# Performance work log

Measured on AMD Instinct MI355X. Metric: run time of the kernel, lower is better.

## Reference

```python
import jax, jax.numpy as jnp
import numpy as np

N = 25000   # num nodes
E = 500000  # num edges
B = 4       # num queries (batch)
D = 32      # hidden dim
R2 = 474    # doubled num_relation
L = 4       # num conv layers
EPS = 1e-6


def setup_inputs() -> dict:
    key = jax.random.key(0)
    ks = jax.random.split(key, 12)
    return {
        "node_in": jax.random.randint(ks[0], (E,), 0, N),
        "node_out": jax.random.randint(ks[1], (E,), 0, N),
        "relation": jax.random.randint(ks[2], (E,), 0, R2),
        "edge_weight": jnp.ones((E,), jnp.float32),
        "h_index": jax.random.randint(ks[3], (B,), 0, N),
        "r_index": jax.random.randint(ks[4], (B,), 0, R2),
        "query_embed": jax.random.normal(ks[5], (R2, D), jnp.float32) * 0.1,
        "rel_W": jax.random.normal(ks[6], (L, D, R2 * D), jnp.float32) * 0.05,
        "rel_b": jnp.zeros((L, R2 * D), jnp.float32),
        "lin_W": jax.random.normal(ks[7], (L, 13 * D, D), jnp.float32) * 0.05,
        "lin_b": jnp.zeros((L, D), jnp.float32),
        "mlp_W1": jax.random.normal(ks[8], (2 * D, 2 * D), jnp.float32) * 0.05,
        "mlp_b1": jnp.zeros((2 * D,), jnp.float32),
        "mlp_W2": jax.random.normal(ks[9], (2 * D, 1), jnp.float32) * 0.05,
        "mlp_b2": jnp.zeros((1,), jnp.float32),
    }


def _nbfnet(node_in, node_out, relation, h_index, r_index,
            edge_weight, query_embed, rel_W, rel_b, lin_W, lin_b,
            mlp_W1, mlp_b1, mlp_W2, mlp_b2):
    query = query_embed[r_index]                                   # [B, D]
    # boundary condition: query embedding placed at the head node of each query
    boundary = jnp.zeros((N, B, D), query.dtype).at[h_index, jnp.arange(B)].set(query)
    # append one self-entry per node (boundary message), as in the torch code
    node_out_ext = jnp.concatenate([node_out, jnp.arange(N)])      # [E+N]
    w_ext = jnp.concatenate([edge_weight, jnp.ones((N,), edge_weight.dtype)])[:, None, None]
    cnt = jax.ops.segment_sum(jnp.ones((E + N,), query.dtype), node_out_ext, N)[:, None, None]
    deg = jax.ops.segment_sum(edge_weight, node_out, N) + 1.0      # degree_out + 1, [N]
    scale = jnp.log(deg)
    scale = scale / scale.mean()
    scales = jnp.stack([jnp.ones_like(scale), scale, 1.0 / jnp.clip(scale, 0.01)], -1)  # [N,3]

    hidden = boundary
    for l in range(L):
        # dependent relation embeddings: [R2, B, D]
        rel_in = (query @ rel_W[l] + rel_b[l]).reshape(B, R2, D).transpose(1, 0, 2)
        # distmult message + boundary self-message: [E+N, B, D]
        msg = jnp.concatenate([rel_in[relation] * hidden[node_in], boundary], 0)
        mw = msg * w_ext
        mean = jax.ops.segment_sum(mw, node_out_ext, N) / cnt
        sq_mean = jax.ops.segment_sum(msg * mw, node_out_ext, N) / cnt
        mx = jax.ops.segment_max(mw, node_out_ext, N)
        mn = jax.ops.segment_min(mw, node_out_ext, N)
        std = jnp.sqrt(jnp.clip(sq_mean - mean * mean, EPS))
        feat = jnp.stack([mean, mx, mn, std], -1).reshape(N, B, 4 * D)   # PNA stats
        update = (feat[..., None] * scales[:, None, None, :]).reshape(N, B, 12 * D)
        hidden = jax.nn.relu(jnp.concatenate([hidden, update], -1) @ lin_W[l] + lin_b[l])

    feat = jnp.concatenate([hidden, jnp.broadcast_to(query[None], (N, B, D))], -1)  # [N,B,2D]
    h1 = jax.nn.relu(feat @ mlp_W1 + mlp_b1)
    score = (h1 @ mlp_W2 + mlp_b2)[..., 0]                          # [N, B]
    return score.T                                                  # [B, N]


def reference(node_in, node_out, relation, edge_weight, h_index, r_index,
              query_embed, rel_W, rel_b, lin_W, lin_b,
              mlp_W1, mlp_b1, mlp_W2, mlp_b2):
    return _nbfnet(node_in, node_out, relation, h_index, r_index,
                   edge_weight, query_embed, rel_W, rel_b, lin_W, lin_b,
                   mlp_W1, mlp_b1, mlp_W2, mlp_b2)
```

## Files before the change

kernel.cpp:

```cpp
#include <hip/hip_runtime.h>
#include <hip/hip_fp16.h>

#define NN  25000
#define EE  500000
#define BB  4
#define DD  32
#define LL  4
#define R2C 474
#define BD  128
#define THD 416
#define EPSF 1e-6f
#define WMH 13312
#define CAP 64

#define NEB    245
#define NWMB   208
#define NRELIN 948
#define NW1P   16

typedef _Float16 half8 __attribute__((ext_vector_type(8)));
typedef float    f32x4 __attribute__((ext_vector_type(4)));

__global__ __launch_bounds__(256) void build_setup_kernel(
    const int* __restrict__ node_in, const int* __restrict__ node_out,
    const int* __restrict__ relation, const float* __restrict__ ew,
    int* __restrict__ cnt, int2* __restrict__ ep,
    const float* __restrict__ linW, _Float16* __restrict__ Wm,
    const int* __restrict__ r_index, const float* __restrict__ qemb,
    const float* __restrict__ relW, const float* __restrict__ relB,
    __half* __restrict__ relIn, float* __restrict__ query,
    const float* __restrict__ W1, _Float16* __restrict__ W1m) {
  const int blk = blockIdx.x;
  const int tid = threadIdx.x;
  if (blk < NEB) {
    int i = blk * 256 + tid;
    if (i >= EE / 8) return;
    const int4*   ni4 = (const int4*)node_in;
    const int4*   no4 = (const int4*)node_out;
    const int4*   rl4 = (const int4*)relation;
    const float4* ew4 = (const float4*)ew;
    int4   noA = no4[2 * i], noB = no4[2 * i + 1];
    int4   niA = ni4[2 * i], niB = ni4[2 * i + 1];
    int4   rlA = rl4[2 * i], rlB = rl4[2 * i + 1];
    float4 ewA = ew4[2 * i], ewB = ew4[2 * i + 1];
    int s0 = atomicAdd(&cnt[noA.x], 1);
    int s1 = atomicAdd(&cnt[noA.y], 1);
    int s2 = atomicAdd(&cnt[noA.z], 1);
    int s3 = atomicAdd(&cnt[noA.w], 1);
    int s4 = atomicAdd(&cnt[noB.x], 1);
    int s5 = atomicAdd(&cnt[noB.y], 1);
    int s6 = atomicAdd(&cnt[noB.z], 1);
    int s7 = atomicAdd(&cnt[noB.w], 1);
    ep[noA.x * CAP + s0] = make_int2(niA.x | (rlA.x << 15), __float_as_int(ewA.x));
    ep[noA.y * CAP + s1] = make_int2(niA.y | (rlA.y << 15), __float_as_int(ewA.y));
    ep[noA.z * CAP + s2] = make_int2(niA.z | (rlA.z << 15), __float_as_int(ewA.z));
    ep[noA.w * CAP + s3] = make_int2(niA.w | (rlA.w << 15), __float_as_int(ewA.w));
    ep[noB.x * CAP + s4] = make_int2(niB.x | (rlB.x << 15), __float_as_int(ewB.x));
    ep[noB.y * CAP + s5] = make_int2(niB.y | (rlB.y << 15), __float_as_int(ewB.y));
    ep[noB.z * CAP + s6] = make_int2(niB.z | (rlB.z << 15), __float_as_int(ewB.z));
    ep[noB.w * CAP + s7] = make_int2(niB.w | (rlB.w << 15), __float_as_int(ewB.w));
  } else if (blk < NEB + NWMB) {
    int idx = (blk - NEB) * 256 + tid;
    int l = idx / WMH, rest = idx % WMH;
    int t = rest >> 10;
    int nt = (rest >> 9) & 1;
    int L = (rest >> 3) & 63;
    int j = rest & 7;
    int k = t * 32 + (L >> 4) * 8 + j;
    int n = nt * 16 + (L & 15);
    int wrow;
    if (k < 32) wrow = k;
    else {
      int kk = k - 32;
      int slab = kk >> 7, s = (kk >> 5) & 3, dd = kk & 31;
      wrow = DD + (dd * 4 + s) * 3 + slab;
    }
    Wm[idx] = (_Float16)linW[(size_t)l * THD * DD + (size_t)wrow * DD + n];
  } else if (blk < NEB + NWMB + NRELIN) {
    int o = (blk - NEB - NWMB) * 256 + tid;
    int l = o / (R2C * BD);
    int rest = o % (R2C * BD);
    int r = rest >> 7, b = (rest >> 5) & 3, d = rest & 31;
    int col = r * DD + d;
    const float* W = relW + (size_t)l * DD * R2C * DD;
    const float* qrow = qemb + (size_t)r_index[b] * DD;
    float acc = relB[(size_t)l * R2C * DD + col];
    #pragma unroll
    for (int k = 0; k < DD; ++k)
      acc = fmaf(qrow[k], W[(size_t)k * (R2C * DD) + col], acc);
    relIn[o] = __float2half(acc);
  } else if (blk < NEB + NWMB + NRELIN + NW1P) {
    int idx = (blk - NEB - NWMB - NRELIN) * 256 + tid;
    int kc = idx >> 11;
    int nt = (idx >> 9) & 3;
    int L = (idx >> 3) & 63;
    int j = idx & 7;
    int k = kc * 32 + (L >> 4) * 8 + j;
    int c = nt * 16 + (L & 15);
    W1m[idx] = (_Float16)W1[(size_t)k * (2 * DD) + c];
  } else {
    if (tid < BD) query[tid] = qemb[(size_t)r_index[tid >> 5] * DD + (tid & 31)];
  }
}

__global__ __launch_bounds__(256) void lg_kernel(const int* __restrict__ cnt,
                                                 const int2* __restrict__ ep,
                                                 float* __restrict__ lg,
                                                 float* __restrict__ logsum) {
  int n = blockIdx.x * 256 + threadIdx.x;
  float v = 0.f;
  if (n < NN) {
    int c = cnt[n];
    const int2* seg = ep + (size_t)n * CAP;
    float s = 0.f;
    for (int i = 0; i < c; ++i) s += __int_as_float(seg[i].y);
    v = logf(s + 1.0f);
    lg[n] = v;
  }
  __shared__ float red[256];
  red[threadIdx.x] = v; __syncthreads();
  for (int o = 128; o > 0; o >>= 1) {
    if (threadIdx.x < o) red[threadIdx.x] += red[threadIdx.x + o];
    __syncthreads();
  }
  if (threadIdx.x == 0) atomicAdd(logsum, red[0]);
}

template <bool LAST>
__device__ __forceinline__ void mfma_epilogue(const _Float16* sh,
                                              const _Float16* hinh,
                                              __half* houth,
                                              const float* lg,
                                              const float* logsum,
                                              const _Float16* Wm,
                                              const float* bias,
                                              const float* query,
                                              const int* h_index,
                                              int nbase, int lane, bool hzero,
                                              const _Float16* W1m,
                                              const float* b1,
                                              const float* W2,
                                              const float* b2,
                                              float* out,
                                              _Float16* hbuf) {
  const int m = lane & 15;
  const int q = lane >> 4;
  const int nl = m >> 2;
  const int n = nbase + nl;
  const int b = m & 3;
  const float sc = lg[n] * ((float)NN / logsum[0]);
  const _Float16 one = (_Float16)1.f;
  const _Float16 s1h = (_Float16)sc;
  const _Float16 s2h = (_Float16)(1.0f / fmaxf(sc, 0.01f));
  const _Float16* ssrc = sh + nl * 512 + b * 32 + q * 8;

  f32x4 c0 = {0.f, 0.f, 0.f, 0.f};
  f32x4 c1 = {0.f, 0.f, 0.f, 0.f};
  half8 a;
  if (hzero) {
    a = (half8)(_Float16)0.f;
    if (n == h_index[b]) {
      const float* qp = query + b * 32 + q * 8;
      #pragma unroll
      for (int j = 0; j < 8; ++j) a[j] = (_Float16)qp[j];
    }
  } else {
    a = *(const half8*)(hinh + (unsigned)n * BD + b * 32 + q * 8);
  }
  #pragma unroll
  for (int t = 0; t < 13; ++t) {
    if (t > 0) {
      const int slab = (t - 1) >> 2, s = (t - 1) & 3;
      a = *(const half8*)(ssrc + s * 128);
      const _Float16 sch = (slab == 0) ? one : ((slab == 1) ? s1h : s2h);
      half8 sv = {sch, sch, sch, sch, sch, sch, sch, sch};
      a = a * sv;
    }
    half8 b0 = *(const half8*)(Wm + (unsigned)(t * 2 + 0) * 512 + lane * 8);
    half8 b1f = *(const half8*)(Wm + (unsigned)(t * 2 + 1) * 512 + lane * 8);
    c0 = __builtin_amdgcn_mfma_f32_16x16x32_f16(a, b0, c0, 0, 0, 0);
    c1 = __builtin_amdgcn_mfma_f32_16x16x32_f16(a, b1f, c1, 0, 0, 0);
  }
  const int col = lane & 15;
  const float bj0 = bias[col], bj1 = bias[col + 16];
  if constexpr (!LAST) {
    #pragma unroll
    for (int i = 0; i < 4; ++i) {
      const int mr = q * 4 + i;
      __half* dst = houth + (unsigned)(nbase + (mr >> 2)) * BD + (mr & 3) * 32 + col;
      dst[0]  = __float2half(fmaxf(c0[i] + bj0, 0.f));
      dst[16] = __float2half(fmaxf(c1[i] + bj1, 0.f));
    }
  } else {
    #pragma unroll
    for (int i = 0; i < 4; ++i) {
      const int mr = q * 4 + i;
      hbuf[mr * 32 + col]      = (_Float16)fmaxf(c0[i] + bj0, 0.f);
      hbuf[mr * 32 + 16 + col] = (_Float16)fmaxf(c1[i] + bj1, 0.f);
    }
    half8 ah = *(const half8*)(hbuf + m * 32 + q * 8);
    half8 aq;
    const float* qp = query + b * 32 + q * 8;
    #pragma unroll
    for (int j = 0; j < 8; ++j) aq[j] = (_Float16)qp[j];
    f32x4 h1c[4];
    #pragma unroll
    for (int nt = 0; nt < 4; ++nt) {
      h1c[nt] = (f32x4){0.f, 0.f, 0.f, 0.f};
      half8 w0 = *(const half8*)(W1m + (unsigned)(0 * 4 + nt) * 512 + lane * 8);
      half8 w1 = *(const half8*)(W1m + (unsigned)(1 * 4 + nt) * 512 + lane * 8);
      h1c[nt] = __builtin_amdgcn_mfma_f32_16x16x32_f16(ah, w0, h1c[nt], 0, 0, 0);
      h1c[nt] = __builtin_amdgcn_mfma_f32_16x16x32_f16(aq, w1, h1c[nt], 0, 0, 0);
    }
    float part[4] = {0.f, 0.f, 0.f, 0.f};
    #pragma unroll
    for (int nt = 0; nt < 4; ++nt) {
      const float bb = b1[nt * 16 + col];
      const float ww = W2[nt * 16 + col];
      #pragma unroll
      for (int i = 0; i < 4; ++i) {
        float v = fmaxf(h1c[nt][i] + bb, 0.f);
        part[i] = fmaf(v, ww, part[i]);
      }
    }
    #pragma unroll
    for (int i = 0; i < 4; ++i) {
      part[i] += __shfl_xor(part[i], 1);
      part[i] += __shfl_xor(part[i], 2);
      part[i] += __shfl_xor(part[i], 4);
      part[i] += __shfl_xor(part[i], 8);
    }
    if (col == 0) {
      const float b2v = b2[0];
      #pragma unroll
      for (int i = 0; i < 4; ++i)
        out[(unsigned)i * NN + nbase + q] = part[i] + b2v;
    }
  }
}

__global__ __launch_bounds__(256) void layer1_fused_kernel(
    const __half2* __restrict__ rel2, const int2* __restrict__ ep,
    const int* __restrict__ cnt, const int* __restrict__ h_index,
    const float* __restrict__ query, const float* __restrict__ lg,
    const float* __restrict__ logsum, const _Float16* __restrict__ Wm,
    const float* __restrict__ bias, __half* __restrict__ houth) {
  __shared__ __align__(16) __half2 sh[4][256];
  const int lane = threadIdx.x & 63;
  const int wid  = threadIdx.x >> 6;
  const int nbase = blockIdx.x * 4;
  const int n = nbase + wid;
  const int b = lane >> 4;
  const int d0 = (lane & 15) * 2;
  const float q0 = query[b * 32 + d0], q1 = query[b * 32 + d0 + 1];
  const int hb = h_index[b];
  const int beg = n * CAP;
  const int cnn = __builtin_amdgcn_readfirstlane(cnt[n]);
  const float mb0 = (n == hb) ? q0 : 0.f;
  const float mb1 = (n == hb) ? q1 : 0.f;
  float sa0 = mb0, qa0 = mb0 * mb0, mx0 = mb0, mn0 = mb0;
  float sa1 = mb1, qa1 = mb1 * mb1, mx1 = mb1, mn1 = mb1;
  int matched = 0;
  for (int p = beg; p < beg + cnn; ++p) {
    int2 e = ep[p];
    if ((e.x & 0x7fff) == hb) {
      __half2 rv = rel2[(unsigned)((unsigned)e.x >> 15) * 64 + lane];
      float w = __int_as_float(e.y);
      float2 rf = __half22float2(rv);
      float m0 = rf.x * q0, mw0 = m0 * w;
      float m1 = rf.y * q1, mw1 = m1 * w;
      sa0 += mw0; qa0 = fmaf(m0, mw0, qa0); mx0 = fmaxf(mx0, mw0); mn0 = fminf(mn0, mw0);
      sa1 += mw1; qa1 = fmaf(m1, mw1, qa1); mx1 = fmaxf(mx1, mw1); mn1 = fminf(mn1, mw1);
      ++matched;
    }
  }
  if (matched < cnn) {
    mx0 = fmaxf(mx0, 0.f); mn0 = fminf(mn0, 0.f);
    mx1 = fmaxf(mx1, 0.f); mn1 = fminf(mn1, 0.f);
  }
  const float invc = 1.0f / (float)(cnn + 1);
  const float mean0 = sa0 * invc, mean1 = sa1 * invc;
  const float sd0 = sqrtf(fmaxf(qa0 * invc - mean0 * mean0, EPSF));
  const float sd1 = sqrtf(fmaxf(qa1 * invc - mean1 * mean1, EPSF));
  sh[wid][lane]       = __floats2half2_rn(mean0, mean1);
  sh[wid][64 + lane]  = __floats2half2_rn(mx0, mx1);
  sh[wid][128 + lane] = __floats2half2_rn(mn0, mn1);
  sh[wid][192 + lane] = __floats2half2_rn(sd0, sd1);
  __syncthreads();
  if (threadIdx.x >= 64) return;
  mfma_epilogue<false>((const _Float16*)&sh[0][0], nullptr, houth, lg, logsum,
                       Wm, bias, query, h_index, nbase, lane, true,
                       nullptr, nullptr, nullptr, nullptr, nullptr, nullptr);
}

template <bool LAST>
__global__ __launch_bounds__(256) void layer_fused_kernel(
    const __half2* __restrict__ hin2, const __half2* __restrict__ rel2,
    const int2* __restrict__ ep, const int* __restrict__ cnt,
    const int* __restrict__ h_index, const float* __restrict__ query,
    const float* __restrict__ lg, const float* __restrict__ logsum,
    const _Float16* __restrict__ Wm, const float* __restrict__ bias,
    __half* __restrict__ houth,
    const _Float16* __restrict__ W1m, const float* __restrict__ b1,
    const float* __restrict__ W2, const float* __restrict__ b2,
    float* __restrict__ out) {
  __shared__ __align__(16) __half2 sh[4][256];
  __shared__ __align__(16) _Float16 hbuf[512];
  const int lane = threadIdx.x & 63;
  const int wid  = threadIdx.x >> 6;
  const int nbase = blockIdx.x * 4;
  const int n = nbase + wid;
  const int b = lane >> 4;
  const int d0 = (lane & 15) * 2;
  const float q0 = query[b * 32 + d0], q1 = query[b * 32 + d0 + 1];
  const int hb = h_index[b];
  const int beg = n * CAP;
  const int cnn = __builtin_amdgcn_readfirstlane(cnt[n]);
  const float mb0 = (n == hb) ? q0 : 0.f;
  const float mb1 = (n == hb) ? q1 : 0.f;
  float sa0 = mb0, qa0 = mb0 * mb0, mx0 = mb0, mn0 = mb0;
  float sa1 = mb1, qa1 = mb1 * mb1, mx1 = mb1, mn1 = mb1;

#define PROC(Ez, Hv, Rv) {                                                   \
    float w = __int_as_float(Ez);                                            \
    float2 hf = __half22float2(Hv), rf = __half22float2(Rv);                 \
    float m0 = rf.x * hf.x, mw0 = m0 * w;                                    \
    float m1 = rf.y * hf.y, mw1 = m1 * w;                                    \
    sa0 += mw0; qa0 = fmaf(m0, mw0, qa0);                                    \
    mx0 = fmaxf(mx0, mw0); mn0 = fminf(mn0, mw0);                            \
    sa1 += mw1; qa1 = fmaf(m1, mw1, qa1);                                    \
    mx1 = fmaxf(mx1, mw1); mn1 = fminf(mn1, mw1); }
#define ROWS(Ex, Hd, Rd) {                                                   \
    Hd = hin2[(unsigned)((Ex) & 0x7fff) * 64 + lane];                        \
    Rd = rel2[(unsigned)((unsigned)(Ex) >> 15) * 64 + lane]; }

  int p = beg;
  int rem = cnn;
  const int nb = rem >> 3;
  if (nb > 0) {
    int2 E0, E1, E2, E3, E4, E5, E6, E7;
    __half2 H0, H1, H2, H3, H4, H5, H6, H7;
    __half2 R0, R1, R2, R3, R4, R5, R6, R7;
    E0 = ep[p];     E1 = ep[p + 1]; E2 = ep[p + 2]; E3 = ep[p + 3];
    E4 = ep[p + 4]; E5 = ep[p + 5]; E6 = ep[p + 6]; E7 = ep[p + 7];
    ROWS(E0.x, H0, R0); ROWS(E1.x, H1, R1); ROWS(E2.x, H2, R2); ROWS(E3.x, H3, R3);
    ROWS(E4.x, H4, R4); ROWS(E5.x, H5, R5); ROWS(E6.x, H6, R6); ROWS(E7.x, H7, R7);
    for (int it = 1; it < nb; ++it) {
      const int pn = p + 8;
      int2 F0 = ep[pn],     F1 = ep[pn + 1], F2 = ep[pn + 2], F3 = ep[pn + 3];
      int2 F4 = ep[pn + 4], F5 = ep[pn + 5], F6 = ep[pn + 6], F7 = ep[pn + 7];
      __half2 G0, G1, G2, G3, G4, G5, G6, G7;
      __half2 S0, S1, S2, S3, S4, S5, S6, S7;
      ROWS(F0.x, G0, S0); ROWS(F1.x, G1, S1); ROWS(F2.x, G2, S2); ROWS(F3.x, G3, S3);
      ROWS(F4.x, G4, S4); ROWS(F5.x, G5, S5); ROWS(F6.x, G6, S6); ROWS(F7.x, G7, S7);
      PROC(E0.y, H0, R0); PROC(E1.y, H1, R1); PROC(E2.y, H2, R2); PROC(E3.y, H3, R3);
      PROC(E4.y, H4, R4); PROC(E5.y, H5, R5); PROC(E6.y, H6, R6); PROC(E7.y, H7, R7);
      E0 = F0; E1 = F1; E2 = F2; E3 = F3; E4 = F4; E5 = F5; E6 = F6; E7 = F7;
      H0 = G0; H1 = G1; H2 = G2; H3 = G3; H4 = G4; H5 = G5; H6 = G6; H7 = G7;
      R0 = S0; R1 = S1; R2 = S2; R3 = S3; R4 = S4; R5 = S5; R6 = S6; R7 = S7;
      p = pn;
    }
    PROC(E0.y, H0, R0); PROC(E1.y, H1, R1); PROC(E2.y, H2, R2); PROC(E3.y, H3, R3);
    PROC(E4.y, H4, R4); PROC(E5.y, H5, R5); PROC(E6.y, H6, R6); PROC(E7.y, H7, R7);
    p += 8;
    rem -= nb << 3;
  }
  if (rem >= 4) {
    int2 E0 = ep[p], E1 = ep[p + 1], E2 = ep[p + 2], E3 = ep[p + 3];
    __half2 H0, H1, H2, H3, R0, R1, R2, R3;
    ROWS(E0.x, H0, R0); ROWS(E1.x, H1, R1); ROWS(E2.x, H2, R2); ROWS(E3.x, H3, R3);
    PROC(E0.y, H0, R0); PROC(E1.y, H1, R1); PROC(E2.y, H2, R2); PROC(E3.y, H3, R3);
    p += 4; rem -= 4;
  }
  for (; rem > 0; --rem, ++p) {
    int2 e = ep[p];
    __half2 hv, rv;
    ROWS(e.x, hv, rv);
    PROC(e.y, hv, rv);
  }
#undef ROWS
#undef PROC
  const float invc = 1.0f / (float)(cnn + 1);
  const float mean0 = sa0 * invc, mean1 = sa1 * invc;
  const float sd0 = sqrtf(fmaxf(qa0 * invc - mean0 * mean0, EPSF));
  const float sd1 = sqrtf(fmaxf(qa1 * invc - mean1 * mean1, EPSF));
  sh[wid][lane]       = __floats2half2_rn(mean0, mean1);
  sh[wid][64 + lane]  = __floats2half2_rn(mx0, mx1);
  sh[wid][128 + lane] = __floats2half2_rn(mn0, mn1);
  sh[wid][192 + lane] = __floats2half2_rn(sd0, sd1);
  __syncthreads();
  if (threadIdx.x >= 64) return;
  mfma_epilogue<LAST>((const _Float16*)&sh[0][0], (const _Float16*)hin2, houth,
                      lg, logsum, Wm, bias, query, h_index, nbase, lane, false,
                      W1m, b1, W2, b2, out, hbuf);
}

extern "C" void kernel_launch(void* const* d_in, const int* in_sizes, int n_in,
                              void* d_out, int out_size, void* d_ws, size_t ws_size,
                              hipStream_t stream) {
  const int*   node_in  = (const int*)d_in[0];
  const int*   node_out = (const int*)d_in[1];
  const int*   relation = (const int*)d_in[2];
  const float* ew       = (const float*)d_in[3];
  const int*   h_index  = (const int*)d_in[4];
  const int*   r_index  = (const int*)d_in[5];
  const float* qemb     = (const float*)d_in[6];
  const float* relW     = (const float*)d_in[7];
  const float* relB     = (const float*)d_in[8];
  const float* linW     = (const float*)d_in[9];
  const float* linB     = (const float*)d_in[10];
  const float* W1       = (const float*)d_in[11];
  const float* b1       = (const float*)d_in[12];
  const float* W2       = (const float*)d_in[13];
  const float* b2       = (const float*)d_in[14];
  float* out = (float*)d_out;

  char* ws = (char*)d_ws;
  size_t off = 0;
  auto alloc = [&](size_t bytes) -> char* {
    char* p = ws + off;
    off += (bytes + 255) & ~(size_t)255;
    return p;
  };
  __half*   h0     = (__half*)  alloc((size_t)NN * BD * 2);
  __half*   h1buf  = (__half*)  alloc((size_t)NN * BD * 2);
  __half*   relIn  = (__half*)  alloc((size_t)LL * R2C * BD * 2);
  _Float16* Wm     = (_Float16*)alloc((size_t)LL * WMH * 2);
  _Float16* W1m    = (_Float16*)alloc((size_t)4096 * 2);
  int2*     ep     = (int2*)    alloc((size_t)NN * CAP * 8);
  int*      cnti   = (int*)     alloc((size_t)NN * 4);
  float*    stats  = (float*)   alloc(256);
  float*    lg     = (float*)   alloc((size_t)NN * 4);
  float*    query  = (float*)   alloc((size_t)BD * 4);

  float* logsum = stats;

  hipMemsetAsync(cnti, 0, (((size_t)NN * 4 + 255) & ~(size_t)255) + 256, stream);

  build_setup_kernel<<<NEB + NWMB + NRELIN + NW1P + 1, 256, 0, stream>>>(
      node_in, node_out, relation, ew, cnti, ep,
      linW, Wm, r_index, qemb, relW, relB, relIn, query, W1, W1m);
  lg_kernel<<<(NN + 255) / 256, 256, 0, stream>>>(cnti, ep, lg, logsum);

  __half* hin = h0; __half* hout = h1buf;
  for (int l = 0; l < LL; ++l) {
    if (l == 0) {
      layer1_fused_kernel<<<NN / 4, 256, 0, stream>>>(
          (const __half2*)relIn, ep, cnti, h_index, query, lg, logsum,
          Wm, linB, hout);
    } else if (l < LL - 1) {
      layer_fused_kernel<false><<<NN / 4, 256, 0, stream>>>(
          (const __half2*)hin, (const __half2*)relIn + (size_t)l * R2C * 64,
          ep, cnti, h_index, query, lg, logsum,
          Wm + (size_t)l * WMH, linB + (size_t)l * DD, hout,
          nullptr, nullptr, nullptr, nullptr, nullptr);
    } else {
      layer_fused_kernel<true><<<NN / 4, 256, 0, stream>>>(
          (const __half2*)hin, (const __half2*)relIn + (size_t)l * R2C * 64,
          ep, cnti, h_index, query, lg, logsum,
          Wm + (size_t)l * WMH, linB + (size_t)l * DD, hout,
          W1m, b1, W2, b2, out);
    }
    __half* tmp = hin; hin = hout; hout = tmp;
  }
}
```

Baseline: 271.4 us.

## Split each node's edge list across two wavefronts and parallelize degree log

The layer kernels now launch 512 threads per block, so two wavefronts share each node's incoming edges (half each). Partial sum, sum-of-squares, max and min are combined through shared memory before the PNA stats and the MFMA epilogue. This halves the serial gather-loop length per wave and raises memory-level parallelism, at the cost of an extra barrier, more shared memory and a half-idle block during the epilogue. The lg kernel also changes to one wavefront per node, reading edge weights in parallel with a shuffle reduction.

```diff
diff --git a/kernel.cpp b/kernel.cpp
--- a/kernel.cpp
+++ b/kernel.cpp
@@ -12,6 +12,7 @@
 #define EPSF 1e-6f
 #define WMH 13312
 #define CAP 64
+#define FINF 3.0e38f
 
 #define NEB    245
 #define NWMB   208
@@ -107,23 +108,21 @@
                                                  const int2* __restrict__ ep,
                                                  float* __restrict__ lg,
                                                  float* __restrict__ logsum) {
-  int n = blockIdx.x * 256 + threadIdx.x;
-  float v = 0.f;
-  if (n < NN) {
-    int c = cnt[n];
-    const int2* seg = ep + (size_t)n * CAP;
-    float s = 0.f;
-    for (int i = 0; i < c; ++i) s += __int_as_float(seg[i].y);
-    v = logf(s + 1.0f);
-    lg[n] = v;
-  }
-  __shared__ float red[256];
-  red[threadIdx.x] = v; __syncthreads();
-  for (int o = 128; o > 0; o >>= 1) {
-    if (threadIdx.x < o) red[threadIdx.x] += red[threadIdx.x + o];
-    __syncthreads();
-  }
-  if (threadIdx.x == 0) atomicAdd(logsum, red[0]);
+  const int lane = threadIdx.x & 63;
+  const int wv = threadIdx.x >> 6;
+  const int n = blockIdx.x * 4 + wv;
+  const int c = cnt[n];
+  int2 e = ep[(size_t)n * CAP + lane];
+  float s = (lane < c) ? __int_as_float(e.y) : 0.f;
+  #pragma unroll
+  for (int o = 32; o > 0; o >>= 1) s += __shfl_xor(s, o, 64);
+  float v = logf(s + 1.0f);
+  if (lane == 0) lg[n] = v;
+  __shared__ float red[4];
+  if (lane == 0) red[wv] = v;
+  __syncthreads();
+  if (threadIdx.x == 0)
+    atomicAdd(logsum, red[0] + red[1] + red[2] + red[3]);
 }
 
 template <bool LAST>
@@ -239,15 +238,20 @@
   }
 }
 
-__global__ __launch_bounds__(256) void layer1_fused_kernel(
+__global__ __launch_bounds__(512) void layer1_fused_kernel(
     const __half2* __restrict__ rel2, const int2* __restrict__ ep,
     const int* __restrict__ cnt, const int* __restrict__ h_index,
     const float* __restrict__ query, const float* __restrict__ lg,
     const float* __restrict__ logsum, const _Float16* __restrict__ Wm,
     const float* __restrict__ bias, __half* __restrict__ houth) {
   __shared__ __align__(16) __half2 sh[4][256];
-  const int lane = threadIdx.x & 63;
-  const int wid  = threadIdx.x >> 6;
+  __shared__ __align__(16) float4 partA[4][64];
+  __shared__ __align__(16) float4 partB[4][64];
+  const int tid  = threadIdx.x;
+  const int lane = tid & 63;
+  const int wv   = tid >> 6;
+  const int wid  = wv & 3;
+  const int hs   = wv >> 2;
   const int nbase = blockIdx.x * 4;
   const int n = nbase + wid;
   const int b = lane >> 4;
@@ -256,12 +260,21 @@
   const int hb = h_index[b];
   const int beg = n * CAP;
   const int cnn = __builtin_amdgcn_readfirstlane(cnt[n]);
-  const float mb0 = (n == hb) ? q0 : 0.f;
-  const float mb1 = (n == hb) ? q1 : 0.f;
-  float sa0 = mb0, qa0 = mb0 * mb0, mx0 = mb0, mn0 = mb0;
-  float sa1 = mb1, qa1 = mb1 * mb1, mx1 = mb1, mn1 = mb1;
+  const int h = cnn >> 1;
+  const int p0 = hs ? (beg + h) : beg;
+  const int my = hs ? (cnn - h) : h;
+  float sa0, qa0, mx0, mn0, sa1, qa1, mx1, mn1;
+  if (hs == 0) {
+    const float mb0 = (n == hb) ? q0 : 0.f;
+    const float mb1 = (n == hb) ? q1 : 0.f;
+    sa0 = mb0; qa0 = mb0 * mb0; mx0 = mb0; mn0 = mb0;
+    sa1 = mb1; qa1 = mb1 * mb1; mx1 = mb1; mn1 = mb1;
+  } else {
+    sa0 = 0.f; qa0 = 0.f; mx0 = -FINF; mn0 = FINF;
+    sa1 = 0.f; qa1 = 0.f; mx1 = -FINF; mn1 = FINF;
+  }
   int matched = 0;
-  for (int p = beg; p < beg + cnn; ++p) {
+  for (int p = p0; p < p0 + my; ++p) {
     int2 e = ep[p];
     if ((e.x & 0x7fff) == hb) {
       __half2 rv = rel2[(unsigned)((unsigned)e.x >> 15) * 64 + lane];
@@ -274,27 +287,38 @@
       ++matched;
     }
   }
-  if (matched < cnn) {
+  if (matched < my) {
     mx0 = fmaxf(mx0, 0.f); mn0 = fminf(mn0, 0.f);
     mx1 = fmaxf(mx1, 0.f); mn1 = fminf(mn1, 0.f);
   }
-  const float invc = 1.0f / (float)(cnn + 1);
-  const float mean0 = sa0 * invc, mean1 = sa1 * invc;
-  const float sd0 = sqrtf(fmaxf(qa0 * invc - mean0 * mean0, EPSF));
-  const float sd1 = sqrtf(fmaxf(qa1 * invc - mean1 * mean1, EPSF));
-  sh[wid][lane]       = __floats2half2_rn(mean0, mean1);
-  sh[wid][64 + lane]  = __floats2half2_rn(mx0, mx1);
-  sh[wid][128 + lane] = __floats2half2_rn(mn0, mn1);
-  sh[wid][192 + lane] = __floats2half2_rn(sd0, sd1);
+  if (hs) {
+    partA[wid][lane] = make_float4(sa0, sa1, qa0, qa1);
+    partB[wid][lane] = make_float4(mx0, mx1, mn0, mn1);
+  }
   __syncthreads();
-  if (threadIdx.x >= 64) return;
-  mfma_epilogue<false>((const _Float16*)&sh[0][0], nullptr, houth, lg, logsum,
-                       Wm, bias, query, h_index, nbase, lane, true,
-                       nullptr, nullptr, nullptr, nullptr, nullptr, nullptr);
+  if (tid < 256) {
+    float4 pa = partA[wid][lane], pb = partB[wid][lane];
+    sa0 += pa.x; sa1 += pa.y; qa0 += pa.z; qa1 += pa.w;
+    mx0 = fmaxf(mx0, pb.x); mx1 = fmaxf(mx1, pb.y);
+    mn0 = fminf(mn0, pb.z); mn1 = fminf(mn1, pb.w);
+    const float invc = 1.0f / (float)(cnn + 1);
+    const float mean0 = sa0 * invc, mean1 = sa1 * invc;
+    const float sd0 = sqrtf(fmaxf(qa0 * invc - mean0 * mean0, EPSF));
+    const float sd1 = sqrtf(fmaxf(qa1 * invc - mean1 * mean1, EPSF));
+    sh[wid][lane]       = __floats2half2_rn(mean0, mean1);
+    sh[wid][64 + lane]  = __floats2half2_rn(mx0, mx1);
+    sh[wid][128 + lane] = __floats2half2_rn(mn0, mn1);
+    sh[wid][192 + lane] = __floats2half2_rn(sd0, sd1);
+  }
+  __syncthreads();
+  if (tid < 64)
+    mfma_epilogue<false>((const _Float16*)&sh[0][0], nullptr, houth, lg, logsum,
+                         Wm, bias, query, h_index, nbase, lane, true,
+                         nullptr, nullptr, nullptr, nullptr, nullptr, nullptr);
 }
 
 template <bool LAST>
-__global__ __launch_bounds__(256) void layer_fused_kernel(
+__global__ __launch_bounds__(512) void layer_fused_kernel(
     const __half2* __restrict__ hin2, const __half2* __restrict__ rel2,
     const int2* __restrict__ ep, const int* __restrict__ cnt,
     const int* __restrict__ h_index, const float* __restrict__ query,
@@ -305,9 +329,14 @@
     const float* __restrict__ W2, const float* __restrict__ b2,
     float* __restrict__ out) {
   __shared__ __align__(16) __half2 sh[4][256];
+  __shared__ __align__(16) float4 partA[4][64];
+  __shared__ __align__(16) float4 partB[4][64];
   __shared__ __align__(16) _Float16 hbuf[512];
-  const int lane = threadIdx.x & 63;
-  const int wid  = threadIdx.x >> 6;
+  const int tid  = threadIdx.x;
+  const int lane = tid & 63;
+  const int wv   = tid >> 6;
+  const int wid  = wv & 3;
+  const int hs   = wv >> 2;
   const int nbase = blockIdx.x * 4;
   const int n = nbase + wid;
   const int b = lane >> 4;
@@ -316,10 +345,19 @@
   const int hb = h_index[b];
   const int beg = n * CAP;
   const int cnn = __builtin_amdgcn_readfirstlane(cnt[n]);
-  const float mb0 = (n == hb) ? q0 : 0.f;
-  const float mb1 = (n == hb) ? q1 : 0.f;
-  float sa0 = mb0, qa0 = mb0 * mb0, mx0 = mb0, mn0 = mb0;
-  float sa1 = mb1, qa1 = mb1 * mb1, mx1 = mb1, mn1 = mb1;
+  const int h = cnn >> 1;
+  int p = hs ? (beg + h) : beg;
+  int rem = hs ? (cnn - h) : h;
+  float sa0, qa0, mx0, mn0, sa1, qa1, mx1, mn1;
+  if (hs == 0) {
+    const float mb0 = (n == hb) ? q0 : 0.f;
+    const float mb1 = (n == hb) ? q1 : 0.f;
+    sa0 = mb0; qa0 = mb0 * mb0; mx0 = mb0; mn0 = mb0;
+    sa1 = mb1; qa1 = mb1 * mb1; mx1 = mb1; mn1 = mb1;
+  } else {
+    sa0 = 0.f; qa0 = 0.f; mx0 = -FINF; mn0 = FINF;
+    sa1 = 0.f; qa1 = 0.f; mx1 = -FINF; mn1 = FINF;
+  }
 
 #define PROC(Ez, Hv, Rv) {                                                   \
     float w = __int_as_float(Ez);                                            \
@@ -334,8 +372,6 @@
     Hd = hin2[(unsigned)((Ex) & 0x7fff) * 64 + lane];                        \
     Rd = rel2[(unsigned)((unsigned)(Ex) >> 15) * 64 + lane]; }
 
-  int p = beg;
-  int rem = cnn;
   const int nb = rem >> 3;
   if (nb > 0) {
     int2 E0, E1, E2, E3, E4, E5, E6, E7;
@@ -380,19 +416,30 @@
   }
 #undef ROWS
 #undef PROC
-  const float invc = 1.0f / (float)(cnn + 1);
-  const float mean0 = sa0 * invc, mean1 = sa1 * invc;
-  const float sd0 = sqrtf(fmaxf(qa0 * invc - mean0 * mean0, EPSF));
-  const float sd1 = sqrtf(fmaxf(qa1 * invc - mean1 * mean1, EPSF));
-  sh[wid][lane]       = __floats2half2_rn(mean0, mean1);
-  sh[wid][64 + lane]  = __floats2half2_rn(mx0, mx1);
-  sh[wid][128 + lane] = __floats2half2_rn(mn0, mn1);
-  sh[wid][192 + lane] = __floats2half2_rn(sd0, sd1);
+  if (hs) {
+    partA[wid][lane] = make_float4(sa0, sa1, qa0, qa1);
+    partB[wid][lane] = make_float4(mx0, mx1, mn0, mn1);
+  }
   __syncthreads();
-  if (threadIdx.x >= 64) return;
-  mfma_epilogue<LAST>((const _Float16*)&sh[0][0], (const _Float16*)hin2, houth,
-                      lg, logsum, Wm, bias, query, h_index, nbase, lane, false,
-                      W1m, b1, W2, b2, out, hbuf);
+  if (tid < 256) {
+    float4 pa = partA[wid][lane], pb = partB[wid][lane];
+    sa0 += pa.x; sa1 += pa.y; qa0 += pa.z; qa1 += pa.w;
+    mx0 = fmaxf(mx0, pb.x); mx1 = fmaxf(mx1, pb.y);
+    mn0 = fminf(mn0, pb.z); mn1 = fminf(mn1, pb.w);
+    const float invc = 1.0f / (float)(cnn + 1);
+    const float mean0 = sa0 * invc, mean1 = sa1 * invc;
+    const float sd0 = sqrtf(fmaxf(qa0 * invc - mean0 * mean0, EPSF));
+    const float sd1 = sqrtf(fmaxf(qa1 * invc - mean1 * mean1, EPSF));
+    sh[wid][lane]       = __floats2half2_rn(mean0, mean1);
+    sh[wid][64 + lane]  = __floats2half2_rn(mx0, mx1);
+    sh[wid][128 + lane] = __floats2half2_rn(mn0, mn1);
+    sh[wid][192 + lane] = __floats2half2_rn(sd0, sd1);
+  }
+  __syncthreads();
+  if (tid < 64)
+    mfma_epilogue<LAST>((const _Float16*)&sh[0][0], (const _Float16*)hin2, houth,
+                        lg, logsum, Wm, bias, query, h_index, nbase, lane, false,
+                        W1m, b1, W2, b2, out, hbuf);
 }
 
 extern "C" void kernel_launch(void* const* d_in, const int* in_sizes, int n_in,
@@ -440,22 +487,22 @@
   build_setup_kernel<<<NEB + NWMB + NRELIN + NW1P + 1, 256, 0, stream>>>(
       node_in, node_out, relation, ew, cnti, ep,
       linW, Wm, r_index, qemb, relW, relB, relIn, query, W1, W1m);
-  lg_kernel<<<(NN + 255) / 256, 256, 0, stream>>>(cnti, ep, lg, logsum);
+  lg_kernel<<<NN / 4, 256, 0, stream>>>(cnti, ep, lg, logsum);
 
   __half* hin = h0; __half* hout = h1buf;
   for (int l = 0; l < LL; ++l) {
     if (l == 0) {
-      layer1_fused_kernel<<<NN / 4, 256, 0, stream>>>(
+      layer1_fused_kernel<<<NN / 4, 512, 0, stream>>>(
           (const __half2*)relIn, ep, cnti, h_index, query, lg, logsum,
           Wm, linB, hout);
     } else if (l < LL - 1) {
-      layer_fused_kernel<false><<<NN / 4, 256, 0, stream>>>(
+      layer_fused_kernel<false><<<NN / 4, 512, 0, stream>>>(
           (const __half2*)hin, (const __half2*)relIn + (size_t)l * R2C * 64,
           ep, cnti, h_index, query, lg, logsum,
           Wm + (size_t)l * WMH, linB + (size_t)l * DD, hout,
           nullptr, nullptr, nullptr, nullptr, nullptr);
     } else {
-      layer_fused_kernel<true><<<NN / 4, 256, 0, stream>>>(
+      layer_fused_kernel<true><<<NN / 4, 512, 0, stream>>>(
           (const __half2*)hin, (const __half2*)relIn + (size_t)l * R2C * 64,
           ep, cnti, h_index, query, lg, logsum,
           Wm + (size_t)l * WMH, linB + (size_t)l * DD, hout,
```

After: 358.1 us. +31.9%, slower.

## Split each node's edges across four lane groups with 16-byte gathers

Applied to the files above, without the earlier changes.

Each wave now processes four edges at once. Its 64 lanes form four groups of 16, and each lane gathers 8 halves (one int4) of the hidden and relation rows. Edge entries are loaded once per lane and broadcast with shuffles, and partial sum, square-sum, max and min are merged across groups with xor shuffles. The lg kernel moves from one thread per node to one wave per node with a shuffle reduction. The aim is fewer, wider memory transactions and more edges in flight per wave, at the cost of extra registers (32 accumulators per lane) and a cross-lane reduction.

```diff
diff --git a/kernel.cpp b/kernel.cpp
--- a/kernel.cpp
+++ b/kernel.cpp
@@ -12,6 +12,7 @@
 #define EPSF 1e-6f
 #define WMH 13312
 #define CAP 64
+#define FINF 3.0e38f
 
 #define NEB    245
 #define NWMB   208
@@ -103,27 +104,35 @@
   }
 }
 
-__global__ __launch_bounds__(256) void lg_kernel(const int* __restrict__ cnt,
-                                                 const int2* __restrict__ ep,
-                                                 float* __restrict__ lg,
-                                                 float* __restrict__ logsum) {
-  int n = blockIdx.x * 256 + threadIdx.x;
-  float v = 0.f;
-  if (n < NN) {
-    int c = cnt[n];
-    const int2* seg = ep + (size_t)n * CAP;
-    float s = 0.f;
-    for (int i = 0; i < c; ++i) s += __int_as_float(seg[i].y);
-    v = logf(s + 1.0f);
-    lg[n] = v;
-  }
-  __shared__ float red[256];
-  red[threadIdx.x] = v; __syncthreads();
-  for (int o = 128; o > 0; o >>= 1) {
-    if (threadIdx.x < o) red[threadIdx.x] += red[threadIdx.x + o];
-    __syncthreads();
-  }
-  if (threadIdx.x == 0) atomicAdd(logsum, red[0]);
+__global__ __launch_bounds__(1024) void lg_kernel(const int* __restrict__ cnt,
+                                                  const int2* __restrict__ ep,
+                                                  float* __restrict__ lg,
+                                                  float* __restrict__ logsum) {
+  const int lane = threadIdx.x & 63;
+  const int wv   = threadIdx.x >> 6;
+  const int nb   = blockIdx.x * 256 + wv * 16;
+  float acc = 0.f;
+  for (int it = 0; it < 16; ++it) {
+    int n = nb + it;
+    if (n < NN) {
+      int c = cnt[n];
+      int2 e = ep[(size_t)n * CAP + lane];
+      float s = (lane < c) ? __int_as_float(e.y) : 0.f;
+      #pragma unroll
+      for (int o = 32; o > 0; o >>= 1) s += __shfl_xor(s, o);
+      float v = logf(s + 1.0f);
+      if (lane == 0) { lg[n] = v; acc += v; }
+    }
+  }
+  __shared__ float red[16];
+  if (lane == 0) red[wv] = acc;
+  __syncthreads();
+  if (threadIdx.x == 0) {
+    float t = 0.f;
+    #pragma unroll
+    for (int i = 0; i < 16; ++i) t += red[i];
+    atomicAdd(logsum, t);
+  }
 }
 
 template <bool LAST>
@@ -240,62 +249,128 @@
 }
 
 __global__ __launch_bounds__(256) void layer1_fused_kernel(
-    const __half2* __restrict__ rel2, const int2* __restrict__ ep,
+    const int4* __restrict__ rel4, const int2* __restrict__ ep,
     const int* __restrict__ cnt, const int* __restrict__ h_index,
     const float* __restrict__ query, const float* __restrict__ lg,
     const float* __restrict__ logsum, const _Float16* __restrict__ Wm,
     const float* __restrict__ bias, __half* __restrict__ houth) {
   __shared__ __align__(16) __half2 sh[4][256];
-  const int lane = threadIdx.x & 63;
-  const int wid  = threadIdx.x >> 6;
+  const int tid = threadIdx.x;
+  const int lane = tid & 63;
+  const int wid = tid >> 6;
+  const int c8 = lane & 15;
+  const int eg = lane >> 4;
   const int nbase = blockIdx.x * 4;
   const int n = nbase + wid;
-  const int b = lane >> 4;
-  const int d0 = (lane & 15) * 2;
-  const float q0 = query[b * 32 + d0], q1 = query[b * 32 + d0 + 1];
-  const int hb = h_index[b];
-  const int beg = n * CAP;
+  const int hb = h_index[c8 >> 2];
   const int cnn = __builtin_amdgcn_readfirstlane(cnt[n]);
-  const float mb0 = (n == hb) ? q0 : 0.f;
-  const float mb1 = (n == hb) ? q1 : 0.f;
-  float sa0 = mb0, qa0 = mb0 * mb0, mx0 = mb0, mn0 = mb0;
-  float sa1 = mb1, qa1 = mb1 * mb1, mx1 = mb1, mn1 = mb1;
+  const int2 myE = ep[n * CAP + lane];
+  const float4* q4 = (const float4*)query;
+  float4 qA = q4[c8 * 2], qB = q4[c8 * 2 + 1];
+  float q8[8] = {qA.x, qA.y, qA.z, qA.w, qB.x, qB.y, qB.z, qB.w};
+  float sa[8], qa[8], mx[8], mn[8];
+  const bool g0 = (eg == 0);
+  const bool head = (n == hb);
+  #pragma unroll
+  for (int j = 0; j < 8; ++j) {
+    float mv = (g0 && head) ? q8[j] : 0.f;
+    sa[j] = mv; qa[j] = mv * mv;
+    mx[j] = g0 ? mv : -FINF;
+    mn[j] = g0 ? mv : FINF;
+  }
   int matched = 0;
-  for (int p = beg; p < beg + cnn; ++p) {
-    int2 e = ep[p];
-    if ((e.x & 0x7fff) == hb) {
-      __half2 rv = rel2[(unsigned)((unsigned)e.x >> 15) * 64 + lane];
-      float w = __int_as_float(e.y);
-      float2 rf = __half22float2(rv);
-      float m0 = rf.x * q0, mw0 = m0 * w;
-      float m1 = rf.y * q1, mw1 = m1 * w;
-      sa0 += mw0; qa0 = fmaf(m0, mw0, qa0); mx0 = fmaxf(mx0, mw0); mn0 = fminf(mn0, mw0);
-      sa1 += mw1; qa1 = fmaf(m1, mw1, qa1); mx1 = fmaxf(mx1, mw1); mn1 = fminf(mn1, mw1);
-      ++matched;
-    }
-  }
+  const int nsf = cnn >> 2;
+  const int tail = cnn & 3;
+  #pragma unroll 2
+  for (int j = 0; j < nsf; ++j) {
+    int sl = j * 4 + eg;
+    int ex = __shfl(myE.x, sl);
+    int ey = __shfl(myE.y, sl);
+    bool mt = ((ex & 0x7fff) == hb);
+    unsigned rr = mt ? ((unsigned)ex >> 15) : 0u;
+    float w = mt ? __int_as_float(ey) : 0.f;
+    int4 Rv = rel4[rr * 16 + c8];
+    const __half2* rp = (const __half2*)&Rv;
+    #pragma unroll
+    for (int u = 0; u < 4; ++u) {
+      float2 rf = __half22float2(rp[u]);
+      float m0 = rf.x * q8[2 * u], m1 = rf.y * q8[2 * u + 1];
+      float w0 = m0 * w, w1 = m1 * w;
+      sa[2 * u] += w0; sa[2 * u + 1] += w1;
+      qa[2 * u] = fmaf(m0, w0, qa[2 * u]);
+      qa[2 * u + 1] = fmaf(m1, w1, qa[2 * u + 1]);
+      mx[2 * u]     = mt ? fmaxf(mx[2 * u], w0)     : mx[2 * u];
+      mn[2 * u]     = mt ? fminf(mn[2 * u], w0)     : mn[2 * u];
+      mx[2 * u + 1] = mt ? fmaxf(mx[2 * u + 1], w1) : mx[2 * u + 1];
+      mn[2 * u + 1] = mt ? fminf(mn[2 * u + 1], w1) : mn[2 * u + 1];
+    }
+    matched += mt ? 1 : 0;
+  }
+  if (tail) {
+    int sl = nsf * 4 + eg;
+    int ex = __shfl(myE.x, sl);
+    int ey = __shfl(myE.y, sl);
+    bool act = eg < tail;
+    bool mt = act && ((ex & 0x7fff) == hb);
+    unsigned rr = mt ? ((unsigned)ex >> 15) : 0u;
+    float w = mt ? __int_as_float(ey) : 0.f;
+    int4 Rv = rel4[rr * 16 + c8];
+    const __half2* rp = (const __half2*)&Rv;
+    #pragma unroll
+    for (int u = 0; u < 4; ++u) {
+      float2 rf = __half22float2(rp[u]);
+      float m0 = rf.x * q8[2 * u], m1 = rf.y * q8[2 * u + 1];
+      float w0 = m0 * w, w1 = m1 * w;
+      sa[2 * u] += w0; sa[2 * u + 1] += w1;
+      qa[2 * u] = fmaf(m0, w0, qa[2 * u]);
+      qa[2 * u + 1] = fmaf(m1, w1, qa[2 * u + 1]);
+      mx[2 * u]     = mt ? fmaxf(mx[2 * u], w0)     : mx[2 * u];
+      mn[2 * u]     = mt ? fminf(mn[2 * u], w0)     : mn[2 * u];
+      mx[2 * u + 1] = mt ? fmaxf(mx[2 * u + 1], w1) : mx[2 * u + 1];
+      mn[2 * u + 1] = mt ? fminf(mn[2 * u + 1], w1) : mn[2 * u + 1];
+    }
+    matched += mt ? 1 : 0;
+  }
+  #pragma unroll
+  for (int j = 0; j < 8; ++j) {
+    sa[j] += __shfl_xor(sa[j], 16);
+    qa[j] += __shfl_xor(qa[j], 16);
+    mx[j] = fmaxf(mx[j], __shfl_xor(mx[j], 16));
+    mn[j] = fminf(mn[j], __shfl_xor(mn[j], 16));
+    sa[j] += __shfl_xor(sa[j], 32);
+    qa[j] += __shfl_xor(qa[j], 32);
+    mx[j] = fmaxf(mx[j], __shfl_xor(mx[j], 32));
+    mn[j] = fminf(mn[j], __shfl_xor(mn[j], 32));
+  }
+  matched += __shfl_xor(matched, 16);
+  matched += __shfl_xor(matched, 32);
   if (matched < cnn) {
-    mx0 = fmaxf(mx0, 0.f); mn0 = fminf(mn0, 0.f);
-    mx1 = fmaxf(mx1, 0.f); mn1 = fminf(mn1, 0.f);
+    #pragma unroll
+    for (int j = 0; j < 8; ++j) {
+      mx[j] = fmaxf(mx[j], 0.f);
+      mn[j] = fminf(mn[j], 0.f);
+    }
   }
   const float invc = 1.0f / (float)(cnn + 1);
-  const float mean0 = sa0 * invc, mean1 = sa1 * invc;
-  const float sd0 = sqrtf(fmaxf(qa0 * invc - mean0 * mean0, EPSF));
-  const float sd1 = sqrtf(fmaxf(qa1 * invc - mean1 * mean1, EPSF));
-  sh[wid][lane]       = __floats2half2_rn(mean0, mean1);
-  sh[wid][64 + lane]  = __floats2half2_rn(mx0, mx1);
-  sh[wid][128 + lane] = __floats2half2_rn(mn0, mn1);
-  sh[wid][192 + lane] = __floats2half2_rn(sd0, sd1);
+  half8 ov;
+  #pragma unroll
+  for (int j = 0; j < 8; ++j) {
+    float mean = sa[j] * invc;
+    float sd = sqrtf(fmaxf(qa[j] * invc - mean * mean, EPSF));
+    float v = (eg == 0) ? mean : ((eg == 1) ? mx[j] : ((eg == 2) ? mn[j] : sd));
+    ov[j] = (_Float16)v;
+  }
+  ((half8*)sh)[wid * 64 + eg * 16 + c8] = ov;
   __syncthreads();
-  if (threadIdx.x >= 64) return;
-  mfma_epilogue<false>((const _Float16*)&sh[0][0], nullptr, houth, lg, logsum,
-                       Wm, bias, query, h_index, nbase, lane, true,
-                       nullptr, nullptr, nullptr, nullptr, nullptr, nullptr);
+  if (tid < 64)
+    mfma_epilogue<false>((const _Float16*)&sh[0][0], nullptr, houth, lg, logsum,
+                         Wm, bias, query, h_index, nbase, lane, true,
+                         nullptr, nullptr, nullptr, nullptr, nullptr, nullptr);
 }
 
 template <bool LAST>
 __global__ __launch_bounds__(256) void layer_fused_kernel(
-    const __half2* __restrict__ hin2, const __half2* __restrict__ rel2,
+    const int4* __restrict__ hin4, const int4* __restrict__ rel4,
     const int2* __restrict__ ep, const int* __restrict__ cnt,
     const int* __restrict__ h_index, const float* __restrict__ query,
     const float* __restrict__ lg, const float* __restrict__ logsum,
@@ -306,93 +381,109 @@
     float* __restrict__ out) {
   __shared__ __align__(16) __half2 sh[4][256];
   __shared__ __align__(16) _Float16 hbuf[512];
-  const int lane = threadIdx.x & 63;
-  const int wid  = threadIdx.x >> 6;
+  const int tid = threadIdx.x;
+  const int lane = tid & 63;
+  const int wid = tid >> 6;
+  const int c8 = lane & 15;
+  const int eg = lane >> 4;
   const int nbase = blockIdx.x * 4;
   const int n = nbase + wid;
-  const int b = lane >> 4;
-  const int d0 = (lane & 15) * 2;
-  const float q0 = query[b * 32 + d0], q1 = query[b * 32 + d0 + 1];
-  const int hb = h_index[b];
-  const int beg = n * CAP;
+  const int hb = h_index[c8 >> 2];
   const int cnn = __builtin_amdgcn_readfirstlane(cnt[n]);
-  const float mb0 = (n == hb) ? q0 : 0.f;
-  const float mb1 = (n == hb) ? q1 : 0.f;
-  float sa0 = mb0, qa0 = mb0 * mb0, mx0 = mb0, mn0 = mb0;
-  float sa1 = mb1, qa1 = mb1 * mb1, mx1 = mb1, mn1 = mb1;
-
-#define PROC(Ez, Hv, Rv) {                                                   \
-    float w = __int_as_float(Ez);                                            \
-    float2 hf = __half22float2(Hv), rf = __half22float2(Rv);                 \
-    float m0 = rf.x * hf.x, mw0 = m0 * w;                                    \
-    float m1 = rf.y * hf.y, mw1 = m1 * w;                                    \
-    sa0 += mw0; qa0 = fmaf(m0, mw0, qa0);                                    \
-    mx0 = fmaxf(mx0, mw0); mn0 = fminf(mn0, mw0);                            \
-    sa1 += mw1; qa1 = fmaf(m1, mw1, qa1);                                    \
-    mx1 = fmaxf(mx1, mw1); mn1 = fminf(mn1, mw1); }
-#define ROWS(Ex, Hd, Rd) {                                                   \
-    Hd = hin2[(unsigned)((Ex) & 0x7fff) * 64 + lane];                        \
-    Rd = rel2[(unsigned)((unsigned)(Ex) >> 15) * 64 + lane]; }
-
-  int p = beg;
-  int rem = cnn;
-  const int nb = rem >> 3;
-  if (nb > 0) {
-    int2 E0, E1, E2, E3, E4, E5, E6, E7;
-    __half2 H0, H1, H2, H3, H4, H5, H6, H7;
-    __half2 R0, R1, R2, R3, R4, R5, R6, R7;
-    E0 = ep[p];     E1 = ep[p + 1]; E2 = ep[p + 2]; E3 = ep[p + 3];
-    E4 = ep[p + 4]; E5 = ep[p + 5]; E6 = ep[p + 6]; E7 = ep[p + 7];
-    ROWS(E0.x, H0, R0); ROWS(E1.x, H1, R1); ROWS(E2.x, H2, R2); ROWS(E3.x, H3, R3);
-    ROWS(E4.x, H4, R4); ROWS(E5.x, H5, R5); ROWS(E6.x, H6, R6); ROWS(E7.x, H7, R7);
-    for (int it = 1; it < nb; ++it) {
-      const int pn = p + 8;
-      int2 F0 = ep[pn],     F1 = ep[pn + 1], F2 = ep[pn + 2], F3 = ep[pn + 3];
-      int2 F4 = ep[pn + 4], F5 = ep[pn + 5], F6 = ep[pn + 6], F7 = ep[pn + 7];
-      __half2 G0, G1, G2, G3, G4, G5, G6, G7;
-      __half2 S0, S1, S2, S3, S4, S5, S6, S7;
-      ROWS(F0.x, G0, S0); ROWS(F1.x, G1, S1); ROWS(F2.x, G2, S2); ROWS(F3.x, G3, S3);
-      ROWS(F4.x, G4, S4); ROWS(F5.x, G5, S5); ROWS(F6.x, G6, S6); ROWS(F7.x, G7, S7);
-      PROC(E0.y, H0, R0); PROC(E1.y, H1, R1); PROC(E2.y, H2, R2); PROC(E3.y, H3, R3);
-      PROC(E4.y, H4, R4); PROC(E5.y, H5, R5); PROC(E6.y, H6, R6); PROC(E7.y, H7, R7);
-      E0 = F0; E1 = F1; E2 = F2; E3 = F3; E4 = F4; E5 = F5; E6 = F6; E7 = F7;
-      H0 = G0; H1 = G1; H2 = G2; H3 = G3; H4 = G4; H5 = G5; H6 = G6; H7 = G7;
-      R0 = S0; R1 = S1; R2 = S2; R3 = S3; R4 = S4; R5 = S5; R6 = S6; R7 = S7;
-      p = pn;
-    }
-    PROC(E0.y, H0, R0); PROC(E1.y, H1, R1); PROC(E2.y, H2, R2); PROC(E3.y, H3, R3);
-    PROC(E4.y, H4, R4); PROC(E5.y, H5, R5); PROC(E6.y, H6, R6); PROC(E7.y, H7, R7);
-    p += 8;
-    rem -= nb << 3;
-  }
-  if (rem >= 4) {
-    int2 E0 = ep[p], E1 = ep[p + 1], E2 = ep[p + 2], E3 = ep[p + 3];
-    __half2 H0, H1, H2, H3, R0, R1, R2, R3;
-    ROWS(E0.x, H0, R0); ROWS(E1.x, H1, R1); ROWS(E2.x, H2, R2); ROWS(E3.x, H3, R3);
-    PROC(E0.y, H0, R0); PROC(E1.y, H1, R1); PROC(E2.y, H2, R2); PROC(E3.y, H3, R3);
-    p += 4; rem -= 4;
-  }
-  for (; rem > 0; --rem, ++p) {
-    int2 e = ep[p];
-    __half2 hv, rv;
-    ROWS(e.x, hv, rv);
-    PROC(e.y, hv, rv);
-  }
-#undef ROWS
-#undef PROC
+  const int2 myE = ep[n * CAP + lane];
+  const float4* q4 = (const float4*)query;
+  float4 qA = q4[c8 * 2], qB = q4[c8 * 2 + 1];
+  float q8[8] = {qA.x, qA.y, qA.z, qA.w, qB.x, qB.y, qB.z, qB.w};
+  float sa[8], qa[8], mx[8], mn[8];
+  const bool g0 = (eg == 0);
+  const bool head = (n == hb);
+  #pragma unroll
+  for (int j = 0; j < 8; ++j) {
+    float mv = (g0 && head) ? q8[j] : 0.f;
+    sa[j] = mv; qa[j] = mv * mv;
+    mx[j] = g0 ? mv : -FINF;
+    mn[j] = g0 ? mv : FINF;
+  }
+  const int nsf = cnn >> 2;
+  const int tail = cnn & 3;
+  #pragma unroll 2
+  for (int j = 0; j < nsf; ++j) {
+    int sl = j * 4 + eg;
+    int ex = __shfl(myE.x, sl);
+    int ey = __shfl(myE.y, sl);
+    int src = ex & 0x7fff;
+    unsigned rr = (unsigned)ex >> 15;
+    float w = __int_as_float(ey);
+    int4 Hv = hin4[(unsigned)src * 16 + c8];
+    int4 Rv = rel4[rr * 16 + c8];
+    const __half2* hp = (const __half2*)&Hv;
+    const __half2* rp = (const __half2*)&Rv;
+    #pragma unroll
+    for (int u = 0; u < 4; ++u) {
+      float2 hf = __half22float2(hp[u]);
+      float2 rf = __half22float2(rp[u]);
+      float m0 = rf.x * hf.x, m1 = rf.y * hf.y;
+      float w0 = m0 * w, w1 = m1 * w;
+      sa[2 * u] += w0; sa[2 * u + 1] += w1;
+      qa[2 * u] = fmaf(m0, w0, qa[2 * u]);
+      qa[2 * u + 1] = fmaf(m1, w1, qa[2 * u + 1]);
+      mx[2 * u] = fmaxf(mx[2 * u], w0);         mn[2 * u] = fminf(mn[2 * u], w0);
+      mx[2 * u + 1] = fmaxf(mx[2 * u + 1], w1); mn[2 * u + 1] = fminf(mn[2 * u + 1], w1);
+    }
+  }
+  if (tail) {
+    int sl = nsf * 4 + eg;
+    int ex = __shfl(myE.x, sl);
+    int ey = __shfl(myE.y, sl);
+    bool act = eg < tail;
+    int src = act ? (ex & 0x7fff) : 0;
+    unsigned rr = act ? ((unsigned)ex >> 15) : 0u;
+    float w = act ? __int_as_float(ey) : 0.f;
+    int4 Hv = hin4[(unsigned)src * 16 + c8];
+    int4 Rv = rel4[rr * 16 + c8];
+    const __half2* hp = (const __half2*)&Hv;
+    const __half2* rp = (const __half2*)&Rv;
+    #pragma unroll
+    for (int u = 0; u < 4; ++u) {
+      float2 hf = __half22float2(hp[u]);
+      float2 rf = __half22float2(rp[u]);
+      float m0 = rf.x * hf.x, m1 = rf.y * hf.y;
+      float w0 = m0 * w, w1 = m1 * w;
+      sa[2 * u] += w0; sa[2 * u + 1] += w1;
+      qa[2 * u] = fmaf(m0, w0, qa[2 * u]);
+      qa[2 * u + 1] = fmaf(m1, w1, qa[2 * u + 1]);
+      mx[2 * u]     = act ? fmaxf(mx[2 * u], w0)     : mx[2 * u];
+      mn[2 * u]     = act ? fminf(mn[2 * u], w0)     : mn[2 * u];
+      mx[2 * u + 1] = act ? fmaxf(mx[2 * u + 1], w1) : mx[2 * u + 1];
+      mn[2 * u + 1] = act ? fminf(mn[2 * u + 1], w1) : mn[2 * u + 1];
+    }
+  }
+  #pragma unroll
+  for (int j = 0; j < 8; ++j) {
+    sa[j] += __shfl_xor(sa[j], 16);
+    qa[j] += __shfl_xor(qa[j], 16);
+    mx[j] = fmaxf(mx[j], __shfl_xor(mx[j], 16));
+    mn[j] = fminf(mn[j], __shfl_xor(mn[j], 16));
+    sa[j] += __shfl_xor(sa[j], 32);
+    qa[j] += __shfl_xor(qa[j], 32);
+    mx[j] = fmaxf(mx[j], __shfl_xor(mx[j], 32));
+    mn[j] = fminf(mn[j], __shfl_xor(mn[j], 32));
+  }
   const float invc = 1.0f / (float)(cnn + 1);
-  const float mean0 = sa0 * invc, mean1 = sa1 * invc;
-  const float sd0 = sqrtf(fmaxf(qa0 * invc - mean0 * mean0, EPSF));
-  const float sd1 = sqrtf(fmaxf(qa1 * invc - mean1 * mean1, EPSF));
-  sh[wid][lane]       = __floats2half2_rn(mean0, mean1);
-  sh[wid][64 + lane]  = __floats2half2_rn(mx0, mx1);
-  sh[wid][128 + lane] = __floats2half2_rn(mn0, mn1);
-  sh[wid][192 + lane] = __floats2half2_rn(sd0, sd1);
+  half8 ov;
+  #pragma unroll
+  for (int j = 0; j < 8; ++j) {
+    float mean = sa[j] * invc;
+    float sd = sqrtf(fmaxf(qa[j] * invc - mean * mean, EPSF));
+    float v = (eg == 0) ? mean : ((eg == 1) ? mx[j] : ((eg == 2) ? mn[j] : sd));
+    ov[j] = (_Float16)v;
+  }
+  ((half8*)sh)[wid * 64 + eg * 16 + c8] = ov;
   __syncthreads();
-  if (threadIdx.x >= 64) return;
-  mfma_epilogue<LAST>((const _Float16*)&sh[0][0], (const _Float16*)hin2, houth,
-                      lg, logsum, Wm, bias, query, h_index, nbase, lane, false,
-                      W1m, b1, W2, b2, out, hbuf);
+  if (tid < 64)
+    mfma_epilogue<LAST>((const _Float16*)&sh[0][0], (const _Float16*)hin4, houth,
+                        lg, logsum, Wm, bias, query, h_index, nbase, lane, false,
+                        W1m, b1, W2, b2, out, hbuf);
 }
 
 extern "C" void kernel_launch(void* const* d_in, const int* in_sizes, int n_in,
@@ -440,23 +531,23 @@
   build_setup_kernel<<<NEB + NWMB + NRELIN + NW1P + 1, 256, 0, stream>>>(
       node_in, node_out, relation, ew, cnti, ep,
       linW, Wm, r_index, qemb, relW, relB, relIn, query, W1, W1m);
-  lg_kernel<<<(NN + 255) / 256, 256, 0, stream>>>(cnti, ep, lg, logsum);
+  lg_kernel<<<98, 1024, 0, stream>>>(cnti, ep, lg, logsum);
 
   __half* hin = h0; __half* hout = h1buf;
   for (int l = 0; l < LL; ++l) {
     if (l == 0) {
       layer1_fused_kernel<<<NN / 4, 256, 0, stream>>>(
-          (const __half2*)relIn, ep, cnti, h_index, query, lg, logsum,
+          (const int4*)relIn, ep, cnti, h_index, query, lg, logsum,
           Wm, linB, hout);
     } else if (l < LL - 1) {
       layer_fused_kernel<false><<<NN / 4, 256, 0, stream>>>(
-          (const __half2*)hin, (const __half2*)relIn + (size_t)l * R2C * 64,
+          (const int4*)hin, (const int4*)relIn + (size_t)l * R2C * 16,
           ep, cnti, h_index, query, lg, logsum,
           Wm + (size_t)l * WMH, linB + (size_t)l * DD, hout,
           nullptr, nullptr, nullptr, nullptr, nullptr);
     } else {
       layer_fused_kernel<true><<<NN / 4, 256, 0, stream>>>(
-          (const __half2*)hin, (const __half2*)relIn + (size_t)l * R2C * 64,
+          (const int4*)hin, (const int4*)relIn + (size_t)l * R2C * 16,
           ep, cnti, h_index, query, lg, logsum,
           Wm + (size_t)l * WMH, linB + (size_t)l * DD, hout,
           W1m, b1, W2, b2, out);
```

Result: slower. 324.4 us (+19.5%).
